# Optimization experiments

Measured on AMD Instinct MI355X. Metric: run time of the kernel, lower is better.

## Reference

```python
import jax, jax.numpy as jnp
import numpy as np

B, H, W, C = 16, 64, 64, 256
C8 = C // 8

def setup_inputs() -> dict:
    key = jax.random.key(0)
    ks = jax.random.split(key, 8)
    return {
        "x": jax.random.normal(ks[0], (B, H, W, C), dtype=jnp.float32),
        "Wf": jax.random.normal(ks[1], (C, C8), dtype=jnp.float32) * 0.05,
        "Wg": jax.random.normal(ks[2], (C, C8), dtype=jnp.float32) * 0.05,
        "Wh": jax.random.normal(ks[3], (C, C), dtype=jnp.float32) * 0.05,
        "bf": jax.random.normal(ks[4], (C8,), dtype=jnp.float32) * 0.05,
        "bg": jax.random.normal(ks[5], (C8,), dtype=jnp.float32) * 0.05,
        "bh": jax.random.normal(ks[6], (C,), dtype=jnp.float32) * 0.05,
        "gamma": jax.random.normal(ks[7], (1,), dtype=jnp.float32) * 0.05,
    }

def reference(x, Wf, Wg, Wh, bf, bg, bh, gamma):
    # 1x1 convs == per-pixel channel matmuls (NHWC)
    f = jnp.einsum('bhwc,cd->bhwd', x, Wf) + bf  # [B,H,W,C/8]
    g = jnp.einsum('bhwc,cd->bhwd', x, Wg) + bg  # [B,H,W,C/8]
    h = jnp.einsum('bhwc,cd->bhwd', x, Wh) + bh  # [B,H,W,C]
    b = x.shape[0]
    # K.batch_flatten flattens all non-batch dims -> attention over BATCH dim
    gf = g.reshape(b, -1)                      # [B, HWC/8]
    ff = f.reshape(b, -1)                      # [B, HWC/8]
    hf = h.reshape(b, -1)                      # [B, HWC]
    s = gf @ ff.T                              # [B, B]
    beta = jax.nn.softmax(s, axis=-1)          # softmax over batch axis
    o = (beta @ hf).reshape(x.shape)           # [B,H,W,C]
    # activation=None -> linear; gamma-scaled residual
    return gamma * o + x
```

## Files before the change

### kernel.cpp

```cpp
#include <hip/hip_runtime.h>

typedef __attribute__((ext_vector_type(4))) float  f4;
typedef __attribute__((ext_vector_type(2))) float  f2;
typedef __attribute__((ext_vector_type(8))) short  short8;
typedef __attribute__((ext_vector_type(4))) float  f32x4;
typedef __attribute__((ext_vector_type(2))) unsigned int u32x2;

static __device__ __forceinline__ unsigned short f2bf(float f) {
    unsigned u = __builtin_bit_cast(unsigned, f);
    unsigned r = (u + 0x7FFFu + ((u >> 16) & 1u)) >> 16;
    return (unsigned short)r;
}
static __device__ __forceinline__ float bf2f(unsigned short h) {
    return __builtin_bit_cast(float, ((unsigned)h) << 16);
}

__global__ __launch_bounds__(256) void k_setup(const float* __restrict__ Wh,
                                               const float* __restrict__ bh,
                                               const float* __restrict__ Wf,
                                               const float* __restrict__ Wg,
                                               const float* __restrict__ gamma,
                                               unsigned short* __restrict__ WhT,
                                               float* __restrict__ gb,
                                               unsigned short* __restrict__ Wfg_hi,
                                               unsigned short* __restrict__ Wfg_lo) {
    __shared__ float T[8 * 260];
    const int t = threadIdx.x, b = blockIdx.x;
    const float g = gamma[0];
    if (b < 32) {
        const int c0 = b * 8;
        const int cr = t >> 5, q = t & 31;
        f4 v0 = *(const f4*)(Wh + (c0 + cr) * 256 + q * 8);
        f4 v1 = *(const f4*)(Wh + (c0 + cr) * 256 + q * 8 + 4);
        *(f4*)(T + cr * 260 + q * 8)     = v0;
        *(f4*)(T + cr * 260 + q * 8 + 4) = v1;
        __syncthreads();
        short8 o;
        #pragma unroll
        for (int j = 0; j < 8; ++j) o[j] = (short)f2bf(g * T[j * 260 + t]);
        *(short8*)(WhT + t * 256 + c0) = o;
    } else {
        gb[t] = g * bh[t];
        const int n = t >> 2, cq = t & 3;
        const float* Wsrc = (n < 32) ? Wf : Wg;
        const int nn = n & 31;
        #pragma unroll
        for (int c8 = 0; c8 < 8; ++c8) {
            short8 h8, l8;
            #pragma unroll
            for (int k = 0; k < 8; ++k) {
                const int c = cq * 64 + c8 * 8 + k;
                const float v = Wsrc[c * 32 + nn];
                const unsigned short h = f2bf(v);
                h8[k] = (short)h;
                l8[k] = (short)f2bf(v - bf2f(h));
            }
            *(short8*)(Wfg_hi + n * 256 + cq * 64 + c8 * 8) = h8;
            *(short8*)(Wfg_lo + n * 256 + cq * 64 + c8 * 8) = l8;
        }
    }
}

__global__ __launch_bounds__(256, 2) void ka(const float* __restrict__ x,
                                             const unsigned short* __restrict__ Wfg_hi,
                                             const unsigned short* __restrict__ Wfg_lo,
                                             const float* __restrict__ bfv,
                                             const float* __restrict__ bgv,
                                             float* __restrict__ s_part) {
    __shared__ __align__(16) unsigned char smem[65536];

    const int t = threadIdx.x, w = t >> 6, l = t & 63;
    const int p = blockIdx.x * 4 + w;

    f4 xr[16];
    #pragma unroll
    for (int j = 0; j < 16; ++j)
        xr[j] = *(const f4*)(x + (((j << 12) + p) << 8) + l * 4);
    #pragma unroll
    for (int j = 0; j < 16; ++j) {
        const int r = j * 4 + w;
        int bo = r * 512 + l * 8;
        bo ^= (r & 7) << 4;
        const unsigned short h0 = f2bf(xr[j][0]), h1 = f2bf(xr[j][1]);
        const unsigned short h2 = f2bf(xr[j][2]), h3 = f2bf(xr[j][3]);
        u32x2 ph, pl;
        ph[0] = ((unsigned)h1 << 16) | h0;
        ph[1] = ((unsigned)h3 << 16) | h2;
        const unsigned short e0 = f2bf(xr[j][0] - bf2f(h0));
        const unsigned short e1 = f2bf(xr[j][1] - bf2f(h1));
        const unsigned short e2 = f2bf(xr[j][2] - bf2f(h2));
        const unsigned short e3 = f2bf(xr[j][3] - bf2f(h3));
        pl[0] = ((unsigned)e1 << 16) | e0;
        pl[1] = ((unsigned)e3 << 16) | e2;
        *(u32x2*)(smem + bo)         = ph;
        *(u32x2*)(smem + 32768 + bo) = pl;
    }
    __syncthreads();

    const int lrow = l & 15;
    const int kfe  = (l >> 4) * 8;
    const int ncol = w * 16 + lrow;
    f32x4 acc[4];
    #pragma unroll
    for (int mt = 0; mt < 4; ++mt) acc[mt] = (f32x4){0.f, 0.f, 0.f, 0.f};

    #pragma unroll
    for (int k0 = 0; k0 < 256; k0 += 32) {
        const short8 bh_ = *(const short8*)(Wfg_hi + ncol * 256 + k0 + kfe);
        const short8 bl_ = *(const short8*)(Wfg_lo + ncol * 256 + k0 + kfe);
        short8 ah[4], al[4];
        #pragma unroll
        for (int mt = 0; mt < 4; ++mt) {
            const int row = mt * 16 + lrow;
            int bo = row * 512 + (k0 + kfe) * 2;
            bo ^= (row & 7) << 4;
            ah[mt] = *(const short8*)(smem + bo);
            al[mt] = *(const short8*)(smem + 32768 + bo);
        }
        #pragma unroll
        for (int mt = 0; mt < 4; ++mt) {
            acc[mt] = __builtin_amdgcn_mfma_f32_16x16x32_bf16(ah[mt], bh_, acc[mt], 0, 0, 0);
            acc[mt] = __builtin_amdgcn_mfma_f32_16x16x32_bf16(al[mt], bh_, acc[mt], 0, 0, 0);
            acc[mt] = __builtin_amdgcn_mfma_f32_16x16x32_bf16(ah[mt], bl_, acc[mt], 0, 0, 0);
        }
    }
    __syncthreads();

    float* FG = (float*)smem;
    const float bias = (ncol < 32) ? bfv[ncol] : bgv[ncol - 32];
    #pragma unroll
    for (int mt = 0; mt < 4; ++mt)
        #pragma unroll
        for (int jj = 0; jj < 4; ++jj) {
            const int row = mt * 16 + (l >> 4) * 4 + jj;
            FG[row * 68 + ncol] = acc[mt][jj] + bias;
        }
    __syncthreads();

    const int si = t >> 4, sj = t & 15;
    float sacc = 0.f;
    #pragma unroll
    for (int q = 0; q < 4; ++q) {
        const float* Gp = FG + (si * 4 + q) * 68 + 32;
        const float* Fp = FG + (sj * 4 + q) * 68;
        #pragma unroll
        for (int d4 = 0; d4 < 8; ++d4) {
            f4 gv = *(const f4*)(Gp + d4 * 4);
            f4 fv = *(const f4*)(Fp + d4 * 4);
            sacc += gv[0] * fv[0] + gv[1] * fv[1] + gv[2] * fv[2] + gv[3] * fv[3];
        }
    }
    s_part[blockIdx.x * 256 + si * 16 + sj] = sacc;
}

__global__ __launch_bounds__(256) void kb1(const float* __restrict__ s_part,
                                           float* __restrict__ s_red) {
    const int t = threadIdx.x, b = blockIdx.x;
    float a = 0.f;
    #pragma unroll
    for (int k = 0; k < 16; ++k) a += s_part[(b * 16 + k) * 256 + t];
    s_red[b * 256 + t] = a;
}

__global__ __launch_bounds__(1024) void kb2(const float* __restrict__ s_red,
                                            float* __restrict__ beta) {
    __shared__ float red[4 * 256];
    __shared__ float srow[256];
    __shared__ float erow[256];
    const int t = threadIdx.x;
    const int pair = t & 255;
    const int qr = t >> 8;
    float a = 0.f;
    #pragma unroll
    for (int b = qr * 16; b < qr * 16 + 16; ++b) a += s_red[b * 256 + pair];
    red[qr * 256 + pair] = a;
    __syncthreads();
    float s = 0.f, e = 0.f;
    if (t < 256) {
        s = red[pair] + red[256 + pair] + red[512 + pair] + red[768 + pair];
        srow[pair] = s;
    }
    __syncthreads();
    if (t < 256) {
        const int i = pair >> 4;
        float m = srow[i * 16];
        #pragma unroll
        for (int j = 1; j < 16; ++j) m = fmaxf(m, srow[i * 16 + j]);
        e = expf(s - m);
        erow[pair] = e;
    }
    __syncthreads();
    if (t < 256) {
        const int i = pair >> 4;
        float sum = 0.f;
        #pragma unroll
        for (int j = 0; j < 16; ++j) sum += erow[i * 16 + j];
        beta[pair] = e / sum;
    }
}

__global__ __launch_bounds__(256, 3) void kc(const float* __restrict__ x,
                                             const unsigned short* __restrict__ WhT,
                                             const float* __restrict__ gb,
                                             const float* __restrict__ beta,
                                             float* __restrict__ out) {
    __shared__ __align__(16) unsigned char smem[34048];
    float* beta_l = (float*)(smem + 33024);

    const int t = threadIdx.x;
    const int w = t >> 6;
    const int l = t & 63;
    const int p0 = blockIdx.x * 4;
    const int p  = p0 + w;
    const int cbase = l * 4;

    f4 xr[16];
    #pragma unroll
    for (int j = 0; j < 16; ++j)
        xr[j] = *(const f4*)(x + (((j << 12) + p) << 8) + cbase);
    if (t < 64) *(f4*)(beta_l + t * 4) = *(const f4*)(beta + t * 4);
    __syncthreads();

    #pragma unroll
    for (int i = 0; i < 16; ++i) {
        f4 bv0 = *(const f4*)(beta_l + i * 16);
        f4 bv1 = *(const f4*)(beta_l + i * 16 + 4);
        f4 bv2 = *(const f4*)(beta_l + i * 16 + 8);
        f4 bv3 = *(const f4*)(beta_l + i * 16 + 12);
        f4 a = {0.f, 0.f, 0.f, 0.f};
        #pragma unroll
        for (int j = 0; j < 4; ++j) {
            a += xr[j]      * bv0[j];
            a += xr[4 + j]  * bv1[j];
            a += xr[8 + j]  * bv2[j];
            a += xr[12 + j] * bv3[j];
        }
        const int r = i * 4 + w;
        int bo = r * 512 + l * 8;
        bo ^= (r & 7) << 4;
        u32x2 packed;
        packed[0] = ((unsigned)f2bf(a[1]) << 16) | f2bf(a[0]);
        packed[1] = ((unsigned)f2bf(a[3]) << 16) | f2bf(a[2]);
        *(u32x2*)(smem + bo) = packed;
    }
    __syncthreads();

    f32x4 acc[4][4];
    #pragma unroll
    for (int mt = 0; mt < 4; ++mt)
        #pragma unroll
        for (int nt = 0; nt < 4; ++nt) acc[mt][nt] = (f32x4){0.f, 0.f, 0.f, 0.f};

    const int n0 = w * 64;
    const int lrow = l & 15;
    const int hi = l >> 4;
    const int kf = hi * 8;
    const unsigned short* wbase = WhT + (n0 + lrow) * 256 + kf;

    short8 bcur[4], bnxt[4];
    #pragma unroll
    for (int nt = 0; nt < 4; ++nt)
        bcur[nt] = *(const short8*)(wbase + nt * 16 * 256);

    #pragma unroll
    for (int ks = 0; ks < 8; ++ks) {
        const int k0 = ks * 32;
        if (ks < 7) {
            #pragma unroll
            for (int nt = 0; nt < 4; ++nt)
                bnxt[nt] = *(const short8*)(wbase + nt * 16 * 256 + k0 + 32);
        }
        short8 af[4];
        #pragma unroll
        for (int mt = 0; mt < 4; ++mt) {
            const int row = mt * 16 + lrow;
            int bo = row * 512 + (k0 + kf) * 2;
            bo ^= (row & 7) << 4;
            af[mt] = *(const short8*)(smem + bo);
        }
        #pragma unroll
        for (int mt = 0; mt < 4; ++mt)
            #pragma unroll
            for (int nt = 0; nt < 4; ++nt)
                acc[mt][nt] = __builtin_amdgcn_mfma_f32_16x16x32_bf16(
                    af[mt], bcur[nt], acc[mt][nt], 0, 0, 0);
        #pragma unroll
        for (int nt = 0; nt < 4; ++nt) bcur[nt] = bnxt[nt];
    }

    float* cst = (float*)smem;
    const f4 gb4 = *(const f4*)(gb + cbase);
    #pragma unroll
    for (int h = 0; h < 2; ++h) {
        __syncthreads();
        #pragma unroll
        for (int mt2 = 0; mt2 < 2; ++mt2) {
            const int mt = h * 2 + mt2;
            #pragma unroll
            for (int nt = 0; nt < 4; ++nt)
                #pragma unroll
                for (int j = 0; j < 4; ++j) {
                    const int rl = mt2 * 16 + hi * 4 + j;
                    cst[rl * 258 + n0 + nt * 16 + lrow] = acc[mt][nt][j];
                }
        }
        __syncthreads();
        #pragma unroll
        for (int rr = 0; rr < 8; ++rr) {
            const int rl = rr * 4 + w;
            const int rg = h * 32 + rl;
            const int i  = rg >> 2, q = rg & 3;
            const int idx = (((i << 12) + p0 + q) << 8) + cbase;
            f4 o = *(const f4*)(cst + rl * 258 + cbase);
            o += gb4 + *(const f4*)(x + idx);
            __builtin_nontemporal_store(o, (f4*)(out + idx));
        }
    }
}

extern "C" void kernel_launch(void* const* d_in, const int* in_sizes, int n_in,
                              void* d_out, int out_size, void* d_ws, size_t ws_size,
                              hipStream_t stream) {
    const float* x     = (const float*)d_in[0];
    const float* Wf    = (const float*)d_in[1];
    const float* Wg    = (const float*)d_in[2];
    const float* Wh    = (const float*)d_in[3];
    const float* bfv   = (const float*)d_in[4];
    const float* bgv   = (const float*)d_in[5];
    const float* bhv   = (const float*)d_in[6];
    const float* gamma = (const float*)d_in[7];
    float* out = (float*)d_out;

    char* ws = (char*)d_ws;
    unsigned short* WhT = (unsigned short*)ws;
    float* gb     = (float*)(ws + 131072);
    float* beta   = (float*)(ws + 132096);
    float* s_part = (float*)(ws + 133120);
    unsigned short* Wfg_hi = (unsigned short*)(ws + 1181696);
    unsigned short* Wfg_lo = (unsigned short*)(ws + 1214464);
    float* s_red  = (float*)(ws + 1181696);

    k_setup<<<dim3(33), dim3(256), 0, stream>>>(Wh, bhv, Wf, Wg, gamma, WhT, gb, Wfg_hi, Wfg_lo);
    ka<<<dim3(1024), dim3(256), 0, stream>>>(x, Wfg_hi, Wfg_lo, bfv, bgv, s_part);
    kb1<<<dim3(64), dim3(256), 0, stream>>>(s_part, s_red);
    kb2<<<dim3(1), dim3(1024), 0, stream>>>(s_red, beta);
    kc<<<dim3(1024), dim3(256), 0, stream>>>(x, WhT, gb, beta, out);
}
```

Baseline: 79.81 us.

## Compute H=x·Wh in attention-score kernel and mix over batch afterward

When the workspace is large enough, the score kernel also computes the per-pixel projection x·Wh with MFMA, reusing the bf16 x tiles it already staged in shared memory, and writes H in bf16 to a 32 MB workspace buffer. The final kernel then only applies the 16x16 beta mixing to H, adds the bias term and the residual, and uses nontemporal stores, so it no longer runs a GEMM after the softmax. This reorders the computation from (beta·x)·Wh to beta·(x·Wh), taking the projection GEMM off the critical path after the softmax. The cost is an extra 32 MB bf16 write and read of H, higher register pressure in the score kernel, and bf16 rounding of H. The old fused path is kept as a fallback for small workspaces.

```diff
diff --git a/kernel.cpp b/kernel.cpp
--- a/kernel.cpp
+++ b/kernel.cpp
@@ -64,9 +64,11 @@
 __global__ __launch_bounds__(256, 2) void ka(const float* __restrict__ x,
                                              const unsigned short* __restrict__ Wfg_hi,
                                              const unsigned short* __restrict__ Wfg_lo,
+                                             const unsigned short* __restrict__ WhT,
                                              const float* __restrict__ bfv,
                                              const float* __restrict__ bgv,
-                                             float* __restrict__ s_part) {
+                                             float* __restrict__ s_part,
+                                             unsigned short* __restrict__ Hb) {
     __shared__ __align__(16) unsigned char smem[65536];
 
     const int t = threadIdx.x, w = t >> 6, l = t & 63;
@@ -98,11 +100,17 @@
     __syncthreads();
 
     const int lrow = l & 15;
-    const int kfe  = (l >> 4) * 8;
+    const int hi4 = l >> 4;
+    const int kfe  = hi4 * 8;
     const int ncol = w * 16 + lrow;
     f32x4 acc[4];
-    #pragma unroll
-    for (int mt = 0; mt < 4; ++mt) acc[mt] = (f32x4){0.f, 0.f, 0.f, 0.f};
+    f32x4 hacc[4][4];
+    #pragma unroll
+    for (int mt = 0; mt < 4; ++mt) {
+        acc[mt] = (f32x4){0.f, 0.f, 0.f, 0.f};
+        #pragma unroll
+        for (int nt = 0; nt < 4; ++nt) hacc[mt][nt] = (f32x4){0.f, 0.f, 0.f, 0.f};
+    }
 
     #pragma unroll
     for (int k0 = 0; k0 < 256; k0 += 32) {
@@ -123,6 +131,33 @@
             acc[mt] = __builtin_amdgcn_mfma_f32_16x16x32_bf16(al[mt], bh_, acc[mt], 0, 0, 0);
             acc[mt] = __builtin_amdgcn_mfma_f32_16x16x32_bf16(ah[mt], bl_, acc[mt], 0, 0, 0);
         }
+        if (Hb) {
+            short8 hb_[4];
+            #pragma unroll
+            for (int nt = 0; nt < 4; ++nt)
+                hb_[nt] = *(const short8*)(WhT + (w * 64 + nt * 16 + lrow) * 256 + k0 + kfe);
+            #pragma unroll
+            for (int mt = 0; mt < 4; ++mt)
+                #pragma unroll
+                for (int nt = 0; nt < 4; ++nt)
+                    hacc[mt][nt] = __builtin_amdgcn_mfma_f32_16x16x32_bf16(
+                        ah[mt], hb_[nt], hacc[mt][nt], 0, 0, 0);
+        }
+    }
+
+    if (Hb) {
+        const size_t pbase = (size_t)blockIdx.x * 4;
+        #pragma unroll
+        for (int mt = 0; mt < 4; ++mt) {
+            const int j = mt * 4 + hi4;
+            #pragma unroll
+            for (int nt = 0; nt < 4; ++nt) {
+                const int d = w * 64 + nt * 16 + lrow;
+                #pragma unroll
+                for (int jj = 0; jj < 4; ++jj)
+                    Hb[((size_t)j * 4096 + pbase + jj) * 256 + d] = f2bf(hacc[mt][nt][jj]);
+            }
+        }
     }
     __syncthreads();
 
@@ -132,7 +167,7 @@
     for (int mt = 0; mt < 4; ++mt)
         #pragma unroll
         for (int jj = 0; jj < 4; ++jj) {
-            const int row = mt * 16 + (l >> 4) * 4 + jj;
+            const int row = mt * 16 + hi4 * 4 + jj;
             FG[row * 68 + ncol] = acc[mt][jj] + bias;
         }
     __syncthreads();
@@ -199,11 +234,119 @@
     }
 }
 
-__global__ __launch_bounds__(256, 3) void kc(const float* __restrict__ x,
-                                             const unsigned short* __restrict__ WhT,
+__global__ __launch_bounds__(256, 4) void kc(const float* __restrict__ x,
+                                             const unsigned short* __restrict__ Hb,
                                              const float* __restrict__ gb,
                                              const float* __restrict__ beta,
                                              float* __restrict__ out) {
+    __shared__ float beta_l[256];
+    const int t = threadIdx.x, w = t >> 6, l = t & 63;
+    const int p = blockIdx.x * 4 + w;
+    const int cb = l * 4;
+
+    if (t < 64) *(f4*)(beta_l + t * 4) = *(const f4*)(beta + t * 4);
+
+    u32x2 hb[16];
+    #pragma unroll
+    for (int j = 0; j < 16; ++j)
+        hb[j] = *(const u32x2*)(Hb + ((size_t)j * 4096 + p) * 256 + cb);
+    __syncthreads();
+
+    f4 acc[16];
+    #pragma unroll
+    for (int i = 0; i < 16; ++i) acc[i] = (f4){0.f, 0.f, 0.f, 0.f};
+
+    #pragma unroll
+    for (int j = 0; j < 16; ++j) {
+        f4 h;
+        h[0] = bf2f((unsigned short)(hb[j][0] & 0xffffu));
+        h[1] = bf2f((unsigned short)(hb[j][0] >> 16));
+        h[2] = bf2f((unsigned short)(hb[j][1] & 0xffffu));
+        h[3] = bf2f((unsigned short)(hb[j][1] >> 16));
+        #pragma unroll
+        for (int i = 0; i < 16; ++i)
+            acc[i] += h * beta_l[i * 16 + j];
+    }
+
+    const f4 gb4 = *(const f4*)(gb + cb);
+    #pragma unroll
+    for (int i = 0; i < 16; ++i) {
+        const int idx = (((i << 12) + p) << 8) + cb;
+        f4 o = acc[i] + gb4 + *(const f4*)(x + idx);
+        __builtin_nontemporal_store(o, (f4*)(out + idx));
+    }
+}
+
+__device__ __forceinline__ void kc_mix(const f4 (&xr)[16], const float* beta_l,
+                                       unsigned char* stage, int w, int l) {
+    #pragma unroll
+    for (int i = 0; i < 16; ++i) {
+        f4 bv0 = *(const f4*)(beta_l + i * 16);
+        f4 bv1 = *(const f4*)(beta_l + i * 16 + 4);
+        f4 bv2 = *(const f4*)(beta_l + i * 16 + 8);
+        f4 bv3 = *(const f4*)(beta_l + i * 16 + 12);
+        f4 a = {0.f, 0.f, 0.f, 0.f};
+        #pragma unroll
+        for (int j = 0; j < 4; ++j) {
+            a += xr[j]      * bv0[j];
+            a += xr[4 + j]  * bv1[j];
+            a += xr[8 + j]  * bv2[j];
+            a += xr[12 + j] * bv3[j];
+        }
+        const int r = i * 4 + w;
+        int bo = r * 512 + l * 8;
+        bo ^= (r & 7) << 4;
+        u32x2 packed;
+        packed[0] = ((unsigned)f2bf(a[1]) << 16) | f2bf(a[0]);
+        packed[1] = ((unsigned)f2bf(a[3]) << 16) | f2bf(a[2]);
+        *(u32x2*)(stage + bo) = packed;
+    }
+}
+
+__device__ __forceinline__ void kc_gemm(f32x4 (&acc)[4][4], const unsigned char* stage,
+                                        const unsigned short* wbase, int lrow, int kf) {
+    #pragma unroll
+    for (int mt = 0; mt < 4; ++mt)
+        #pragma unroll
+        for (int nt = 0; nt < 4; ++nt) acc[mt][nt] = (f32x4){0.f, 0.f, 0.f, 0.f};
+
+    short8 bcur[4], bnxt[4];
+    #pragma unroll
+    for (int nt = 0; nt < 4; ++nt)
+        bcur[nt] = *(const short8*)(wbase + nt * 16 * 256);
+
+    #pragma unroll
+    for (int ks = 0; ks < 8; ++ks) {
+        const int k0 = ks * 32;
+        if (ks < 7) {
+            #pragma unroll
+            for (int nt = 0; nt < 4; ++nt)
+                bnxt[nt] = *(const short8*)(wbase + nt * 16 * 256 + k0 + 32);
+        }
+        short8 af[4];
+        #pragma unroll
+        for (int mt = 0; mt < 4; ++mt) {
+            const int row = mt * 16 + lrow;
+            int bo = row * 512 + (k0 + kf) * 2;
+            bo ^= (row & 7) << 4;
+            af[mt] = *(const short8*)(stage + bo);
+        }
+        #pragma unroll
+        for (int mt = 0; mt < 4; ++mt)
+            #pragma unroll
+            for (int nt = 0; nt < 4; ++nt)
+                acc[mt][nt] = __builtin_amdgcn_mfma_f32_16x16x32_bf16(
+                    af[mt], bcur[nt], acc[mt][nt], 0, 0, 0);
+        #pragma unroll
+        for (int nt = 0; nt < 4; ++nt) bcur[nt] = bnxt[nt];
+    }
+}
+
+__global__ __launch_bounds__(256, 3) void kc_fused(const float* __restrict__ x,
+                                                   const unsigned short* __restrict__ WhT,
+                                                   const float* __restrict__ gb,
+                                                   const float* __restrict__ beta,
+                                                   float* __restrict__ out) {
     __shared__ __align__(16) unsigned char smem[34048];
     float* beta_l = (float*)(smem + 33024);
 
@@ -213,80 +356,24 @@
     const int p0 = blockIdx.x * 4;
     const int p  = p0 + w;
     const int cbase = l * 4;
-
-    f4 xr[16];
-    #pragma unroll
-    for (int j = 0; j < 16; ++j)
-        xr[j] = *(const f4*)(x + (((j << 12) + p) << 8) + cbase);
-    if (t < 64) *(f4*)(beta_l + t * 4) = *(const f4*)(beta + t * 4);
-    __syncthreads();
-
-    #pragma unroll
-    for (int i = 0; i < 16; ++i) {
-        f4 bv0 = *(const f4*)(beta_l + i * 16);
-        f4 bv1 = *(const f4*)(beta_l + i * 16 + 4);
-        f4 bv2 = *(const f4*)(beta_l + i * 16 + 8);
-        f4 bv3 = *(const f4*)(beta_l + i * 16 + 12);
-        f4 a = {0.f, 0.f, 0.f, 0.f};
-        #pragma unroll
-        for (int j = 0; j < 4; ++j) {
-            a += xr[j]      * bv0[j];
-            a += xr[4 + j]  * bv1[j];
-            a += xr[8 + j]  * bv2[j];
-            a += xr[12 + j] * bv3[j];
-        }
-        const int r = i * 4 + w;
-        int bo = r * 512 + l * 8;
-        bo ^= (r & 7) << 4;
-        u32x2 packed;
-        packed[0] = ((unsigned)f2bf(a[1]) << 16) | f2bf(a[0]);
-        packed[1] = ((unsigned)f2bf(a[3]) << 16) | f2bf(a[2]);
-        *(u32x2*)(smem + bo) = packed;
-    }
-    __syncthreads();
-
-    f32x4 acc[4][4];
-    #pragma unroll
-    for (int mt = 0; mt < 4; ++mt)
-        #pragma unroll
-        for (int nt = 0; nt < 4; ++nt) acc[mt][nt] = (f32x4){0.f, 0.f, 0.f, 0.f};
-
     const int n0 = w * 64;
     const int lrow = l & 15;
     const int hi = l >> 4;
     const int kf = hi * 8;
     const unsigned short* wbase = WhT + (n0 + lrow) * 256 + kf;
 
-    short8 bcur[4], bnxt[4];
-    #pragma unroll
-    for (int nt = 0; nt < 4; ++nt)
-        bcur[nt] = *(const short8*)(wbase + nt * 16 * 256);
-
-    #pragma unroll
-    for (int ks = 0; ks < 8; ++ks) {
-        const int k0 = ks * 32;
-        if (ks < 7) {
-            #pragma unroll
-            for (int nt = 0; nt < 4; ++nt)
-                bnxt[nt] = *(const short8*)(wbase + nt * 16 * 256 + k0 + 32);
-        }
-        short8 af[4];
-        #pragma unroll
-        for (int mt = 0; mt < 4; ++mt) {
-            const int row = mt * 16 + lrow;
-            int bo = row * 512 + (k0 + kf) * 2;
-            bo ^= (row & 7) << 4;
-            af[mt] = *(const short8*)(smem + bo);
-        }
-        #pragma unroll
-        for (int mt = 0; mt < 4; ++mt)
-            #pragma unroll
-            for (int nt = 0; nt < 4; ++nt)
-                acc[mt][nt] = __builtin_amdgcn_mfma_f32_16x16x32_bf16(
-                    af[mt], bcur[nt], acc[mt][nt], 0, 0, 0);
-        #pragma unroll
-        for (int nt = 0; nt < 4; ++nt) bcur[nt] = bnxt[nt];
-    }
+    f4 xr[16];
+    #pragma unroll
+    for (int j = 0; j < 16; ++j)
+        xr[j] = *(const f4*)(x + (((j << 12) + p) << 8) + cbase);
+    if (t < 64) *(f4*)(beta_l + t * 4) = *(const f4*)(beta + t * 4);
+    __syncthreads();
+
+    kc_mix(xr, beta_l, smem, w, l);
+    __syncthreads();
+
+    f32x4 acc[4][4];
+    kc_gemm(acc, smem, wbase, lrow, kf);
 
     float* cst = (float*)smem;
     const f4 gb4 = *(const f4*)(gb + cbase);
@@ -339,10 +426,19 @@
     unsigned short* Wfg_hi = (unsigned short*)(ws + 1181696);
     unsigned short* Wfg_lo = (unsigned short*)(ws + 1214464);
     float* s_red  = (float*)(ws + 1181696);
+    unsigned short* Hbuf = (unsigned short*)(ws + 2097152);
+
+    const bool big_ws = (ws_size >= 2097152ull + 33554432ull);
+    unsigned short* HbArg = big_ws ? Hbuf : nullptr;
 
     k_setup<<<dim3(33), dim3(256), 0, stream>>>(Wh, bhv, Wf, Wg, gamma, WhT, gb, Wfg_hi, Wfg_lo);
-    ka<<<dim3(1024), dim3(256), 0, stream>>>(x, Wfg_hi, Wfg_lo, bfv, bgv, s_part);
+    ka<<<dim3(1024), dim3(256), 0, stream>>>(x, Wfg_hi, Wfg_lo, WhT, bfv, bgv, s_part, HbArg);
     kb1<<<dim3(64), dim3(256), 0, stream>>>(s_part, s_red);
     kb2<<<dim3(1), dim3(1024), 0, stream>>>(s_red, beta);
-    kc<<<dim3(1024), dim3(256), 0, stream>>>(x, WhT, gb, beta, out);
-}
+
+    if (big_ws) {
+        kc<<<dim3(1024), dim3(256), 0, stream>>>(x, Hbuf, gb, beta, out);
+    } else {
+        kc_fused<<<dim3(1024), dim3(256), 0, stream>>>(x, WhT, gb, beta, out);
+    }
+}
```

Measured after the change: 116.7 us. +46.2%, slower.
